# Performance work log

Measured on AMD Instinct MI355X. Metric: run time of the kernel, lower is better.

The kernel has to match this reference:

```python
import jax, jax.numpy as jnp
import numpy as np

B, T, H = 4, 2048, 1024
NH = 16
HD = H // NH  # 64
FF = 4 * H


def setup_inputs() -> dict:
    key = jax.random.key(0)
    ks = jax.random.split(key, 11)
    s = 0.02
    return {
        "x": jax.random.normal(ks[0], (B, T, H), dtype=jnp.float32),
        "Wq": jax.random.normal(ks[1], (H, H), dtype=jnp.float32) * s,
        "bq": jnp.zeros((H,), dtype=jnp.float32),
        "Wk": jax.random.normal(ks[2], (H, H), dtype=jnp.float32) * s,
        "bk": jnp.zeros((H,), dtype=jnp.float32),
        "Wv": jax.random.normal(ks[3], (H, H), dtype=jnp.float32) * s,
        "bv": jnp.zeros((H,), dtype=jnp.float32),
        "W1": jax.random.normal(ks[4], (H, FF), dtype=jnp.float32) * s,
        "b1": jnp.zeros((FF,), dtype=jnp.float32),
        "W2": jax.random.normal(ks[5], (FF, H), dtype=jnp.float32) * s,
        "b2": jnp.zeros((H,), dtype=jnp.float32),
    }


def _block(x, Wq, bq, Wk, bk, Wv, bv, W1, b1, W2, b2):
    b, t, h = x.shape
    # multi-head masked self-attention; NOTE: scale = full h_dim ** 0.5 (as in source)
    q = (x @ Wq + bq).reshape(b, t, NH, HD).transpose(0, 2, 1, 3)  # [B,nH,T,HD]
    k = (x @ Wk + bk).reshape(b, t, NH, HD).transpose(0, 2, 1, 3)
    v = (x @ Wv + bv).reshape(b, t, NH, HD).transpose(0, 2, 1, 3)
    att = jnp.einsum("bnqd,bnkd->bnqk", q, k) / (h ** 0.5)  # [B,nH,T,T]
    causal = jnp.tril(jnp.ones((t, t), dtype=bool))
    att = jnp.where(causal, att, -jnp.inf)
    w = jax.nn.softmax(att, axis=-1)
    attn_out = jnp.einsum("bnqk,bnkd->bnqd", w, v).transpose(0, 2, 1, 3).reshape(b, t, h)
    x = x + attn_out
    # MLP (dropout p=0 -> identity)
    mlp = jax.nn.gelu(x @ W1 + b1) @ W2 + b2
    return x + mlp


def reference(x, Wq, bq, Wk, bk, Wv, bv, W1, b1, W2, b2):
    return _block(x, Wq, bq, Wk, bk, Wv, bv, W1, b1, W2, b2)
```

## Files before the change

kernel.cpp:

```cpp
#include <hip/hip_runtime.h>
#include <cstdint>
#include <cstddef>

typedef unsigned short u16;
typedef __attribute__((ext_vector_type(8))) __bf16 bf16x8;
typedef __attribute__((ext_vector_type(4))) __bf16 bf16x4;
typedef __attribute__((ext_vector_type(4))) float f32x4;
typedef __attribute__((ext_vector_type(4))) u16 u16x4;

#define MFMA(a, b, c) __builtin_amdgcn_mfma_f32_16x16x32_bf16((a), (b), (c), 0, 0, 0)

__device__ __forceinline__ u16 f2b(float f) {
  union { __bf16 h; u16 u; } v;
  v.h = (__bf16)f;
  return v.u;
}

__device__ __forceinline__ void gld16(const void* g, void* l) {
  __builtin_amdgcn_global_load_lds(
      (__attribute__((address_space(1))) void*)(void*)(g),
      (__attribute__((address_space(3))) void*)(l), 16, 0, 0);
}

__device__ __forceinline__ size_t qk_off(int t, int hd) {
  return (size_t)((((t >> 4) * 2 + (hd >> 5)) * 512)
                  + ((((hd >> 3) & 3) * 16 + (t & 15)) * 8) + (hd & 7));
}
__device__ __forceinline__ size_t v_off(int t, int hd) {
  int kk = ((t & 15) << 2) | ((t >> 4) & 3);
  return (size_t)(((t >> 6) * 4096)
                  + (((hd >> 4) * 2 + (kk >> 5)) * 512)
                  + ((((kk >> 3) & 3) * 16 + (hd & 15)) * 8) + (kk & 7));
}

__global__ void xconv(const float* __restrict__ in, u16* __restrict__ out, int n) {
  int i = (blockIdx.x * blockDim.x + threadIdx.x) * 4;
  if (i >= n) return;
  float4 v = *(const float4*)(in + i);
  u16x4 o;
  o[0] = f2b(v.x); o[1] = f2b(v.y); o[2] = f2b(v.z); o[3] = f2b(v.w);
  *(u16x4*)(out + i) = o;
}

__global__ void wtrans_all(const float* __restrict__ Wq, const float* __restrict__ Wk,
                           const float* __restrict__ Wv, const float* __restrict__ W1,
                           const float* __restrict__ W2, u16* __restrict__ Wqkvt,
                           u16* __restrict__ W1t, u16* __restrict__ W2t) {
  __shared__ float tile[32][33];
  int blk = blockIdx.x;
  const float* W;
  u16* Wt;
  int Kd, Nd, nx;
  if (blk < 3072) {
    int s = blk >> 10;
    blk &= 1023;
    W = (s == 0) ? Wq : (s == 1) ? Wk : Wv;
    Wt = Wqkvt + (size_t)s * 1048576;
    Kd = 1024; Nd = 1024; nx = 32;
  } else if (blk < 7168) {
    blk -= 3072; W = W1; Wt = W1t; Kd = 1024; Nd = 4096; nx = 128;
  } else {
    blk -= 7168; W = W2; Wt = W2t; Kd = 4096; Nd = 1024; nx = 32;
  }
  int n0 = (blk % nx) * 32, k0 = (blk / nx) * 32;
  int tx = threadIdx.x, ty = threadIdx.y;
#pragma unroll
  for (int i = 0; i < 4; i++)
    tile[ty + i * 8][tx] = W[(size_t)(k0 + ty + i * 8) * Nd + n0 + tx];
  __syncthreads();
#pragma unroll
  for (int i = 0; i < 4; i++)
    Wt[(size_t)(n0 + ty + i * 8) * Kd + k0 + tx] = f2b(tile[tx][ty + i * 8]);
}

template <int MODE>
__global__ __launch_bounds__(512, 2) void gemm256(
    const u16* __restrict__ A, const u16* __restrict__ Bt,
    const float* __restrict__ b0, const float* __restrict__ b1,
    const float* __restrict__ b2, void* __restrict__ outp,
    const float* __restrict__ resid, int N, int K, float scale) {
  __shared__ __attribute__((aligned(16))) u16 As_[3][16384];
  __shared__ __attribute__((aligned(16))) u16 Bs_[3][8192];
  const int tid = threadIdx.x;
  const int wid = tid >> 6, lane = tid & 63;
  const int g = lane >> 4, r = lane & 15;

  const int xcd = blockIdx.x & 7;
  const int ii = blockIdx.x >> 3;
  const int bm = xcd * 4 + ((ii & 31) >> 3);
  const int bn = (ii >> 5) * 8 + (ii & 7);

  const int wrow = (wid >> 1) * 64;
  const int wcol = (wid & 1) * 64;

  const int ko0 = ((0 * 4 + g) ^ (r & 7)) * 8;
  const int ko1 = ((1 * 4 + g) ^ (r & 7)) * 8;

  size_t aOff[4], bOff[2];
#pragma unroll
  for (int i4 = 0; i4 < 4; i4++) {
    int cc = i4 * 512 + tid, row = cc >> 3;
    int js = ((cc & 7) ^ (row & 7)) * 8;
    aOff[i4] = (size_t)(bm * 256 + row) * K + js;
  }
#pragma unroll
  for (int i2 = 0; i2 < 2; i2++) {
    int cc = i2 * 512 + tid, row = cc >> 3;
    int js = ((cc & 7) ^ (row & 7)) * 8;
    bOff[i2] = (size_t)(bn * 128 + row) * K + js;
  }

  f32x4 acc[4][4];
  const f32x4 zero4 = {0.f, 0.f, 0.f, 0.f};
#pragma unroll
  for (int i = 0; i < 4; i++)
#pragma unroll
    for (int j = 0; j < 4; j++) acc[i][j] = zero4;

#pragma unroll
  for (int i4 = 0; i4 < 4; i4++) gld16(A + aOff[i4], &As_[0][(i4 * 512 + tid) * 8]);
#pragma unroll
  for (int i2 = 0; i2 < 2; i2++) gld16(Bt + bOff[i2], &Bs_[0][(i2 * 512 + tid) * 8]);
#pragma unroll
  for (int i4 = 0; i4 < 4; i4++) gld16(A + aOff[i4] + 64, &As_[1][(i4 * 512 + tid) * 8]);
#pragma unroll
  for (int i2 = 0; i2 < 2; i2++) gld16(Bt + bOff[i2] + 64, &Bs_[1][(i2 * 512 + tid) * 8]);
  asm volatile("s_waitcnt vmcnt(6)" ::: "memory");
  __builtin_amdgcn_s_barrier();

  const int KT = K >> 6;
  int cur = 0;
  for (int t = 0; t < KT; ++t) {
    const u16* as = As_[cur];
    const u16* bs = Bs_[cur];
    const int stg = (cur == 0) ? 2 : cur - 1;
    const bool more = (t + 2) < KT;
    const size_t k2 = (size_t)(t + 2) * 64;

    bf16x8 af0[4], bf0[4], af1[4], bf1[4];
#pragma unroll
    for (int mt = 0; mt < 4; mt++) {
      af0[mt] = *(const bf16x8*)&as[(wrow + mt * 16 + r) * 64 + ko0];
      af1[mt] = *(const bf16x8*)&as[(wrow + mt * 16 + r) * 64 + ko1];
    }
#pragma unroll
    for (int nt = 0; nt < 4; nt++) {
      bf0[nt] = *(const bf16x8*)&bs[(wcol + nt * 16 + r) * 64 + ko0];
      bf1[nt] = *(const bf16x8*)&bs[(wcol + nt * 16 + r) * 64 + ko1];
    }

    if (more) {
#pragma unroll
      for (int i4 = 0; i4 < 4; i4++)
        gld16(A + aOff[i4] + k2, &As_[stg][(i4 * 512 + tid) * 8]);
#pragma unroll
      for (int i2 = 0; i2 < 2; i2++)
        gld16(Bt + bOff[i2] + k2, &Bs_[stg][(i2 * 512 + tid) * 8]);
    }

#pragma unroll
    for (int mt = 0; mt < 4; mt++)
#pragma unroll
      for (int nt = 0; nt < 4; nt++)
        acc[mt][nt] = MFMA(af0[mt], bf0[nt], acc[mt][nt]);
#pragma unroll
    for (int mt = 0; mt < 4; mt++)
#pragma unroll
      for (int nt = 0; nt < 4; nt++)
        acc[mt][nt] = MFMA(af1[mt], bf1[nt], acc[mt][nt]);

    if (t + 1 < KT) {
      if (more) asm volatile("s_waitcnt vmcnt(6)" ::: "memory");
      else      asm volatile("s_waitcnt vmcnt(0)" ::: "memory");
    }
    __builtin_amdgcn_s_barrier();
    cur = (cur == 2) ? 0 : cur + 1;
  }

#pragma unroll
  for (int mt = 0; mt < 4; mt++) {
#pragma unroll
    for (int nt = 0; nt < 4; nt++) {
      int col = bn * 128 + wcol + nt * 16 + r;
      float bv;
      if (MODE == 4) {
        int sec = col >> 10, hcol = col & 1023;
        bv = (sec == 0) ? b0[hcol] : (sec == 1) ? b1[hcol] : b2[hcol];
      } else {
        bv = b0[col];
      }
#pragma unroll
      for (int q = 0; q < 4; q++) {
        int row = bm * 256 + wrow + mt * 16 + g * 4 + q;
        float v = acc[mt][nt][q] + bv;
        if (MODE == 2) {
          const float c1 = -2.3025850929940457f;
          const float c2 = c1 * 0.044715f;
          float t2 = v * v;
          float z = v * (c1 + c2 * t2);
          float sg = 1.0f / (1.0f + __builtin_amdgcn_exp2f(z));
          ((u16*)outp)[(size_t)row * N + col] = f2b(v * sg);
        } else if (MODE == 3) {
          ((float*)outp)[(size_t)row * N + col] = v + resid[(size_t)row * N + col];
        } else if (MODE == 4) {
          int sec = col >> 10, hcol = col & 1023;
          int head = hcol >> 6, hd = hcol & 63;
          int bb = row >> 11, tt = row & 2047;
          size_t hbase = ((size_t)bb * 16 + head) * 131072;
          u16* qout = (u16*)outp;
          if (sec == 0) {
            qout[hbase + qk_off(tt, hd)] = f2b(v * scale);
          } else if (sec == 1) {
            (qout + 8388608)[hbase + qk_off(tt, hd)] = f2b(v);
          } else {
            (qout + 16777216)[hbase + v_off(tt, hd)] = f2b(v);
          }
        }
      }
    }
  }
}

__global__ __launch_bounds__(256) void attn_kernel(
    const u16* __restrict__ Q, const u16* __restrict__ Kc,
    const u16* __restrict__ Vt, const float* __restrict__ x,
    float* __restrict__ x1, u16* __restrict__ xb1) {
  const int bh = blockIdx.x & 63;
  const int slot = blockIdx.x >> 6;
  const int tid = threadIdx.x;
  const int wid = tid >> 6, lane = tid & 63;
  const int g = lane >> 4, c = lane & 15;
  const u16* Qh = Q + (size_t)bh * 131072;
  const u16* Kh = Kc + (size_t)bh * 131072;
  const u16* Vh = Vt + (size_t)bh * 131072;
  const int b = bh >> 4, head = bh & 15;

  __shared__ __attribute__((aligned(16))) u16 Ks[8192];
  __shared__ __attribute__((aligned(16))) u16 Vs[8192];
  __shared__ __attribute__((aligned(16))) u16 P[4][32][72];

  bf16x8 ones;
#pragma unroll
  for (int i = 0; i < 8; i++) ones[i] = (__bf16)1.0f;

  const f32x4 zero4 = {0.f, 0.f, 0.f, 0.f};

  for (int phase = 0; phase < 2; ++phase) {
    const int bt = phase ? (15 - slot) : slot;
    const int q0b = bt * 128;
    const int q0 = q0b + wid * 32;
    const int kendw = q0 + 32;
    const int nkt = bt + 1;

    bf16x8 qf[2][2];
#pragma unroll
    for (int mt = 0; mt < 2; mt++)
#pragma unroll
      for (int h = 0; h < 2; h++)
        qf[mt][h] = *(const bf16x8*)&Qh[(((q0 >> 4) + mt) * 2 + h) * 512 + lane * 8];

    f32x4 o[2][4];
    f32x4 lac[2];
#pragma unroll
    for (int mt = 0; mt < 2; mt++) {
      lac[mt] = zero4;
#pragma unroll
      for (int i = 0; i < 4; i++) o[mt][i] = zero4;
    }

    for (int kt = 0; kt < nkt; ++kt) {
      const int k0 = kt * 128;
#pragma unroll
      for (int r2 = 0; r2 < 4; r2++) {
        int idx = (r2 * 256 + tid) * 8;
        gld16(Kh + (size_t)k0 * 64 + idx, Ks + idx);
        gld16(Vh + (size_t)k0 * 64 + idx, Vs + idx);
      }
      __syncthreads();

#pragma unroll
      for (int s2 = 0; s2 < 2; ++s2) {
        const int k0s = k0 + s2 * 64;
        if (k0s < kendw) {
          bf16x8 kf[4][2], vf[4][2];
#pragma unroll
          for (int nt = 0; nt < 4; nt++)
#pragma unroll
            for (int h = 0; h < 2; h++) {
              kf[nt][h] = *(const bf16x8*)&Ks[s2 * 4096 + (nt * 2 + h) * 512 + lane * 8];
              vf[nt][h] = *(const bf16x8*)&Vs[s2 * 4096 + (nt * 2 + h) * 512 + lane * 8];
            }

          f32x4 sv[2][4];
#pragma unroll
          for (int mt = 0; mt < 2; mt++)
#pragma unroll
            for (int nt = 0; nt < 4; nt++) sv[mt][nt] = zero4;
#pragma unroll
          for (int nt = 0; nt < 4; nt++)
#pragma unroll
            for (int mt = 0; mt < 2; mt++) {
              sv[mt][nt] = MFMA(qf[mt][0], kf[nt][0], sv[mt][nt]);
              sv[mt][nt] = MFMA(qf[mt][1], kf[nt][1], sv[mt][nt]);
            }

          if (k0s + 64 > q0) {
#pragma unroll
            for (int mt = 0; mt < 2; mt++)
#pragma unroll
              for (int rr = 0; rr < 4; rr++) {
                int q = q0 + mt * 16 + g * 4 + rr;
#pragma unroll
                for (int nt = 0; nt < 4; nt++)
                  if (k0s + nt * 16 + c > q) sv[mt][nt][rr] = -1e30f;
              }
          }

#pragma unroll
          for (int mt = 0; mt < 2; mt++)
#pragma unroll
            for (int rr = 0; rr < 4; rr++) {
              union { u16x4 u; bf16x4 h; } pw;
#pragma unroll
              for (int nt = 0; nt < 4; nt++)
                pw.h[nt] = (__bf16)__builtin_amdgcn_exp2f(sv[mt][nt][rr]);
              *(u16x4*)&P[wid][mt * 16 + g * 4 + rr][4 * c] = pw.u;
            }

          asm volatile("s_waitcnt lgkmcnt(0)" ::: "memory");

#pragma unroll
          for (int mt = 0; mt < 2; mt++) {
            bf16x8 pf0 = *(const bf16x8*)&P[wid][mt * 16 + c][g * 8];
            bf16x8 pf1 = *(const bf16x8*)&P[wid][mt * 16 + c][32 + g * 8];
            lac[mt] = MFMA(pf0, ones, lac[mt]);
            lac[mt] = MFMA(pf1, ones, lac[mt]);
#pragma unroll
            for (int ot = 0; ot < 4; ot++) {
              f32x4 oo = MFMA(pf0, vf[ot][0], o[mt][ot]);
              o[mt][ot] = MFMA(pf1, vf[ot][1], oo);
            }
          }
        }
      }
      __syncthreads();
    }

    float inv[2][4];
#pragma unroll
    for (int mt = 0; mt < 2; mt++)
#pragma unroll
      for (int rr = 0; rr < 4; rr++) inv[mt][rr] = 1.0f / lac[mt][rr];
#pragma unroll
    for (int mt = 0; mt < 2; mt++)
#pragma unroll
      for (int ot = 0; ot < 4; ot++)
#pragma unroll
        for (int rr = 0; rr < 4; rr++) {
          int t = q0 + mt * 16 + g * 4 + rr;
          int hd = ot * 16 + c;
          size_t xi = ((size_t)b * 2048 + t) * 1024 + head * 64 + hd;
          float v = x[xi] + o[mt][ot][rr] * inv[mt][rr];
          x1[xi] = v;
          xb1[xi] = f2b(v);
        }
  }
}

extern "C" void kernel_launch(void* const* d_in, const int* in_sizes, int n_in,
                              void* d_out, int out_size, void* d_ws, size_t ws_size,
                              hipStream_t stream) {
  (void)in_sizes; (void)n_in; (void)out_size; (void)ws_size;
  const float* x = (const float*)d_in[0];
  const float* Wq = (const float*)d_in[1];
  const float* bq = (const float*)d_in[2];
  const float* Wk = (const float*)d_in[3];
  const float* bk = (const float*)d_in[4];
  const float* Wv = (const float*)d_in[5];
  const float* bv = (const float*)d_in[6];
  const float* W1 = (const float*)d_in[7];
  const float* b1 = (const float*)d_in[8];
  const float* W2 = (const float*)d_in[9];
  const float* b2 = (const float*)d_in[10];

  char* ws = (char*)d_ws;
  size_t off = 0;
  auto alloc = [&](size_t bytes) {
    char* p = ws + off;
    off += (bytes + 255) & ~(size_t)255;
    return p;
  };
  u16* xb    = (u16*)alloc(8192ull * 1024 * 2);
  u16* Wqkvt = (u16*)alloc(3072ull * 1024 * 2);
  u16* W1t   = (u16*)alloc(4096ull * 1024 * 2);
  u16* W2t   = (u16*)alloc(1024ull * 4096 * 2);
  u16* Qb    = (u16*)alloc(3ull * 8192 * 1024 * 2);
  float* x1  = (float*)alloc(8192ull * 1024 * 4);
  u16* hb    = (u16*)alloc(8192ull * 4096 * 2);
  u16* xb1   = xb;
  u16* Kb    = Qb + 8388608;
  u16* Vtb   = Qb + 16777216;

  const float qscale = 1.4426950408889634f / 32.0f;

  xconv<<<dim3(8192), dim3(256), 0, stream>>>(x, xb, 8192 * 1024);
  wtrans_all<<<dim3(11264), dim3(32, 8), 0, stream>>>(
      Wq, Wk, Wv, W1, W2, Wqkvt, W1t, W2t);
  gemm256<4><<<dim3(768), dim3(512), 0, stream>>>(
      xb, Wqkvt, bq, bk, bv, Qb, nullptr, 3072, 1024, qscale);
  attn_kernel<<<dim3(512), dim3(256), 0, stream>>>(Qb, Kb, Vtb, x, x1, xb1);
  gemm256<2><<<dim3(1024), dim3(512), 0, stream>>>(
      xb1, W1t, b1, nullptr, nullptr, hb, nullptr, 4096, 1024, 1.0f);
  gemm256<3><<<dim3(256), dim3(512), 0, stream>>>(
      hb, W2t, b2, nullptr, nullptr, d_out, x1, 1024, 4096, 1.0f);
}
```

Baseline: 429.3 us.

## Use 256x256 tiles with double buffering for QKV and W1 GEMMs

Adds a gemm_big kernel with 256x256 output tiles per block (8 waves, each computing 128x64) instead of 256x128, halving the block count for the QKV and MLP-up GEMMs. Each block reuses more of every loaded A and B tile, which cuts LDS and global traffic per FLOP. The three-stage prefetch is replaced by two-stage double buffering, with the next A and B loads issued between the two k-halves. The trade-offs are more accumulator registers (128 per thread), less prefetch depth, a full vmcnt(0) wait each iteration, and fewer blocks to fill the CUs. The W2 GEMM keeps the old kernel.

```diff
diff --git a/kernel.cpp b/kernel.cpp
--- a/kernel.cpp
+++ b/kernel.cpp
@@ -74,58 +74,51 @@
 }
 
 template <int MODE>
-__global__ __launch_bounds__(512, 2) void gemm256(
+__global__ __launch_bounds__(512, 2) void gemm_big(
     const u16* __restrict__ A, const u16* __restrict__ Bt,
     const float* __restrict__ b0, const float* __restrict__ b1,
     const float* __restrict__ b2, void* __restrict__ outp,
-    const float* __restrict__ resid, int N, int K, float scale) {
-  __shared__ __attribute__((aligned(16))) u16 As_[3][16384];
-  __shared__ __attribute__((aligned(16))) u16 Bs_[3][8192];
+    int N, int K, float scale) {
+  __shared__ __attribute__((aligned(16))) u16 As_[2][16384];
+  __shared__ __attribute__((aligned(16))) u16 Bs_[2][16384];
   const int tid = threadIdx.x;
   const int wid = tid >> 6, lane = tid & 63;
   const int g = lane >> 4, r = lane & 15;
 
   const int xcd = blockIdx.x & 7;
   const int ii = blockIdx.x >> 3;
-  const int bm = xcd * 4 + ((ii & 31) >> 3);
-  const int bn = (ii >> 5) * 8 + (ii & 7);
-
-  const int wrow = (wid >> 1) * 64;
-  const int wcol = (wid & 1) * 64;
+  const int c4 = ii >> 4, w = ii & 15;
+  const int bm = xcd * 4 + (w >> 2);
+  const int bn = c4 * 4 + (w & 3);
+
+  const int wrow = (wid >> 2) * 128;
+  const int wcol = (wid & 3) * 64;
 
   const int ko0 = ((0 * 4 + g) ^ (r & 7)) * 8;
   const int ko1 = ((1 * 4 + g) ^ (r & 7)) * 8;
 
-  size_t aOff[4], bOff[2];
+  size_t aOff[4], bOff[4];
 #pragma unroll
   for (int i4 = 0; i4 < 4; i4++) {
     int cc = i4 * 512 + tid, row = cc >> 3;
     int js = ((cc & 7) ^ (row & 7)) * 8;
     aOff[i4] = (size_t)(bm * 256 + row) * K + js;
-  }
-#pragma unroll
-  for (int i2 = 0; i2 < 2; i2++) {
-    int cc = i2 * 512 + tid, row = cc >> 3;
-    int js = ((cc & 7) ^ (row & 7)) * 8;
-    bOff[i2] = (size_t)(bn * 128 + row) * K + js;
-  }
-
-  f32x4 acc[4][4];
+    bOff[i4] = (size_t)(bn * 256 + row) * K + js;
+  }
+
+  f32x4 acc[8][4];
   const f32x4 zero4 = {0.f, 0.f, 0.f, 0.f};
 #pragma unroll
-  for (int i = 0; i < 4; i++)
+  for (int i = 0; i < 8; i++)
 #pragma unroll
     for (int j = 0; j < 4; j++) acc[i][j] = zero4;
 
 #pragma unroll
-  for (int i4 = 0; i4 < 4; i4++) gld16(A + aOff[i4], &As_[0][(i4 * 512 + tid) * 8]);
-#pragma unroll
-  for (int i2 = 0; i2 < 2; i2++) gld16(Bt + bOff[i2], &Bs_[0][(i2 * 512 + tid) * 8]);
-#pragma unroll
-  for (int i4 = 0; i4 < 4; i4++) gld16(A + aOff[i4] + 64, &As_[1][(i4 * 512 + tid) * 8]);
-#pragma unroll
-  for (int i2 = 0; i2 < 2; i2++) gld16(Bt + bOff[i2] + 64, &Bs_[1][(i2 * 512 + tid) * 8]);
-  asm volatile("s_waitcnt vmcnt(6)" ::: "memory");
+  for (int i4 = 0; i4 < 4; i4++) {
+    gld16(A + aOff[i4], &As_[0][(i4 * 512 + tid) * 8]);
+    gld16(Bt + bOff[i4], &Bs_[0][(i4 * 512 + tid) * 8]);
+  }
+  asm volatile("s_waitcnt vmcnt(0)" ::: "memory");
   __builtin_amdgcn_s_barrier();
 
   const int KT = K >> 6;
@@ -133,55 +126,64 @@
   for (int t = 0; t < KT; ++t) {
     const u16* as = As_[cur];
     const u16* bs = Bs_[cur];
-    const int stg = (cur == 0) ? 2 : cur - 1;
-    const bool more = (t + 2) < KT;
-    const size_t k2 = (size_t)(t + 2) * 64;
-
-    bf16x8 af0[4], bf0[4], af1[4], bf1[4];
-#pragma unroll
-    for (int mt = 0; mt < 4; mt++) {
-      af0[mt] = *(const bf16x8*)&as[(wrow + mt * 16 + r) * 64 + ko0];
-      af1[mt] = *(const bf16x8*)&as[(wrow + mt * 16 + r) * 64 + ko1];
-    }
+    const int nxt = cur ^ 1;
+    const bool more = (t + 1) < KT;
+    const size_t k1 = (size_t)(t + 1) * 64;
+
+    if (more) {
+#pragma unroll
+      for (int i4 = 0; i4 < 4; i4++)
+        gld16(A + aOff[i4] + k1, &As_[nxt][(i4 * 512 + tid) * 8]);
+    }
+
+    {
+      bf16x8 af[8], bf[4];
+#pragma unroll
+      for (int mt = 0; mt < 8; mt++)
+        af[mt] = *(const bf16x8*)&as[(wrow + mt * 16 + r) * 64 + ko0];
+#pragma unroll
+      for (int nt = 0; nt < 4; nt++)
+        bf[nt] = *(const bf16x8*)&bs[(wcol + nt * 16 + r) * 64 + ko0];
+#pragma unroll
+      for (int mt = 0; mt < 8; mt++)
+#pragma unroll
+        for (int nt = 0; nt < 4; nt++)
+          acc[mt][nt] = MFMA(af[mt], bf[nt], acc[mt][nt]);
+    }
+
+    if (more) {
+#pragma unroll
+      for (int i4 = 0; i4 < 4; i4++)
+        gld16(Bt + bOff[i4] + k1, &Bs_[nxt][(i4 * 512 + tid) * 8]);
+    }
+
+    {
+      bf16x8 af[8], bf[4];
+#pragma unroll
+      for (int mt = 0; mt < 8; mt++)
+        af[mt] = *(const bf16x8*)&as[(wrow + mt * 16 + r) * 64 + ko1];
+#pragma unroll
+      for (int nt = 0; nt < 4; nt++)
+        bf[nt] = *(const bf16x8*)&bs[(wcol + nt * 16 + r) * 64 + ko1];
+#pragma unroll
+      for (int mt = 0; mt < 8; mt++)
+#pragma unroll
+        for (int nt = 0; nt < 4; nt++)
+          acc[mt][nt] = MFMA(af[mt], bf[nt], acc[mt][nt]);
+    }
+
+    if (more) {
+      asm volatile("s_waitcnt vmcnt(0)" ::: "memory");
+      __builtin_amdgcn_s_barrier();
+    }
+    cur = nxt;
+  }
+
+#pragma unroll
+  for (int mt = 0; mt < 8; mt++) {
 #pragma unroll
     for (int nt = 0; nt < 4; nt++) {
-      bf0[nt] = *(const bf16x8*)&bs[(wcol + nt * 16 + r) * 64 + ko0];
-      bf1[nt] = *(const bf16x8*)&bs[(wcol + nt * 16 + r) * 64 + ko1];
-    }
-
-    if (more) {
-#pragma unroll
-      for (int i4 = 0; i4 < 4; i4++)
-        gld16(A + aOff[i4] + k2, &As_[stg][(i4 * 512 + tid) * 8]);
-#pragma unroll
-      for (int i2 = 0; i2 < 2; i2++)
-        gld16(Bt + bOff[i2] + k2, &Bs_[stg][(i2 * 512 + tid) * 8]);
-    }
-
-#pragma unroll
-    for (int mt = 0; mt < 4; mt++)
-#pragma unroll
-      for (int nt = 0; nt < 4; nt++)
-        acc[mt][nt] = MFMA(af0[mt], bf0[nt], acc[mt][nt]);
-#pragma unroll
-    for (int mt = 0; mt < 4; mt++)
-#pragma unroll
-      for (int nt = 0; nt < 4; nt++)
-        acc[mt][nt] = MFMA(af1[mt], bf1[nt], acc[mt][nt]);
-
-    if (t + 1 < KT) {
-      if (more) asm volatile("s_waitcnt vmcnt(6)" ::: "memory");
-      else      asm volatile("s_waitcnt vmcnt(0)" ::: "memory");
-    }
-    __builtin_amdgcn_s_barrier();
-    cur = (cur == 2) ? 0 : cur + 1;
-  }
-
-#pragma unroll
-  for (int mt = 0; mt < 4; mt++) {
-#pragma unroll
-    for (int nt = 0; nt < 4; nt++) {
-      int col = bn * 128 + wcol + nt * 16 + r;
+      int col = bn * 256 + wcol + nt * 16 + r;
       float bv;
       if (MODE == 4) {
         int sec = col >> 10, hcol = col & 1023;
@@ -200,8 +202,6 @@
           float z = v * (c1 + c2 * t2);
           float sg = 1.0f / (1.0f + __builtin_amdgcn_exp2f(z));
           ((u16*)outp)[(size_t)row * N + col] = f2b(v * sg);
-        } else if (MODE == 3) {
-          ((float*)outp)[(size_t)row * N + col] = v + resid[(size_t)row * N + col];
         } else if (MODE == 4) {
           int sec = col >> 10, hcol = col & 1023;
           int head = hcol >> 6, hd = hcol & 63;
@@ -215,6 +215,127 @@
           } else {
             (qout + 16777216)[hbase + v_off(tt, hd)] = f2b(v);
           }
+        }
+      }
+    }
+  }
+}
+
+template <int MODE>
+__global__ __launch_bounds__(512, 2) void gemm256(
+    const u16* __restrict__ A, const u16* __restrict__ Bt,
+    const float* __restrict__ b0, void* __restrict__ outp,
+    const float* __restrict__ resid, int N, int K) {
+  __shared__ __attribute__((aligned(16))) u16 As_[3][16384];
+  __shared__ __attribute__((aligned(16))) u16 Bs_[3][8192];
+  const int tid = threadIdx.x;
+  const int wid = tid >> 6, lane = tid & 63;
+  const int g = lane >> 4, r = lane & 15;
+
+  const int xcd = blockIdx.x & 7;
+  const int ii = blockIdx.x >> 3;
+  const int bm = xcd * 4 + ((ii & 31) >> 3);
+  const int bn = (ii >> 5) * 8 + (ii & 7);
+
+  const int wrow = (wid >> 1) * 64;
+  const int wcol = (wid & 1) * 64;
+
+  const int ko0 = ((0 * 4 + g) ^ (r & 7)) * 8;
+  const int ko1 = ((1 * 4 + g) ^ (r & 7)) * 8;
+
+  size_t aOff[4], bOff[2];
+#pragma unroll
+  for (int i4 = 0; i4 < 4; i4++) {
+    int cc = i4 * 512 + tid, row = cc >> 3;
+    int js = ((cc & 7) ^ (row & 7)) * 8;
+    aOff[i4] = (size_t)(bm * 256 + row) * K + js;
+  }
+#pragma unroll
+  for (int i2 = 0; i2 < 2; i2++) {
+    int cc = i2 * 512 + tid, row = cc >> 3;
+    int js = ((cc & 7) ^ (row & 7)) * 8;
+    bOff[i2] = (size_t)(bn * 128 + row) * K + js;
+  }
+
+  f32x4 acc[4][4];
+  const f32x4 zero4 = {0.f, 0.f, 0.f, 0.f};
+#pragma unroll
+  for (int i = 0; i < 4; i++)
+#pragma unroll
+    for (int j = 0; j < 4; j++) acc[i][j] = zero4;
+
+#pragma unroll
+  for (int i4 = 0; i4 < 4; i4++) gld16(A + aOff[i4], &As_[0][(i4 * 512 + tid) * 8]);
+#pragma unroll
+  for (int i2 = 0; i2 < 2; i2++) gld16(Bt + bOff[i2], &Bs_[0][(i2 * 512 + tid) * 8]);
+#pragma unroll
+  for (int i4 = 0; i4 < 4; i4++) gld16(A + aOff[i4] + 64, &As_[1][(i4 * 512 + tid) * 8]);
+#pragma unroll
+  for (int i2 = 0; i2 < 2; i2++) gld16(Bt + bOff[i2] + 64, &Bs_[1][(i2 * 512 + tid) * 8]);
+  asm volatile("s_waitcnt vmcnt(6)" ::: "memory");
+  __builtin_amdgcn_s_barrier();
+
+  const int KT = K >> 6;
+  int cur = 0;
+  for (int t = 0; t < KT; ++t) {
+    const u16* as = As_[cur];
+    const u16* bs = Bs_[cur];
+    const int stg = (cur == 0) ? 2 : cur - 1;
+    const bool more = (t + 2) < KT;
+    const size_t k2 = (size_t)(t + 2) * 64;
+
+    bf16x8 af0[4], bf0[4], af1[4], bf1[4];
+#pragma unroll
+    for (int mt = 0; mt < 4; mt++) {
+      af0[mt] = *(const bf16x8*)&as[(wrow + mt * 16 + r) * 64 + ko0];
+      af1[mt] = *(const bf16x8*)&as[(wrow + mt * 16 + r) * 64 + ko1];
+    }
+#pragma unroll
+    for (int nt = 0; nt < 4; nt++) {
+      bf0[nt] = *(const bf16x8*)&bs[(wcol + nt * 16 + r) * 64 + ko0];
+      bf1[nt] = *(const bf16x8*)&bs[(wcol + nt * 16 + r) * 64 + ko1];
+    }
+
+    if (more) {
+#pragma unroll
+      for (int i4 = 0; i4 < 4; i4++)
+        gld16(A + aOff[i4] + k2, &As_[stg][(i4 * 512 + tid) * 8]);
+#pragma unroll
+      for (int i2 = 0; i2 < 2; i2++)
+        gld16(Bt + bOff[i2] + k2, &Bs_[stg][(i2 * 512 + tid) * 8]);
+    }
+
+#pragma unroll
+    for (int mt = 0; mt < 4; mt++)
+#pragma unroll
+      for (int nt = 0; nt < 4; nt++)
+        acc[mt][nt] = MFMA(af0[mt], bf0[nt], acc[mt][nt]);
+#pragma unroll
+    for (int mt = 0; mt < 4; mt++)
+#pragma unroll
+      for (int nt = 0; nt < 4; nt++)
+        acc[mt][nt] = MFMA(af1[mt], bf1[nt], acc[mt][nt]);
+
+    if (t + 1 < KT) {
+      if (more) asm volatile("s_waitcnt vmcnt(6)" ::: "memory");
+      else      asm volatile("s_waitcnt vmcnt(0)" ::: "memory");
+    }
+    __builtin_amdgcn_s_barrier();
+    cur = (cur == 2) ? 0 : cur + 1;
+  }
+
+#pragma unroll
+  for (int mt = 0; mt < 4; mt++) {
+#pragma unroll
+    for (int nt = 0; nt < 4; nt++) {
+      int col = bn * 128 + wcol + nt * 16 + r;
+      float bv = b0[col];
+#pragma unroll
+      for (int q = 0; q < 4; q++) {
+        int row = bm * 256 + wrow + mt * 16 + g * 4 + q;
+        float v = acc[mt][nt][q] + bv;
+        if (MODE == 3) {
+          ((float*)outp)[(size_t)row * N + col] = v + resid[(size_t)row * N + col];
         }
       }
     }
@@ -406,11 +527,11 @@
   xconv<<<dim3(8192), dim3(256), 0, stream>>>(x, xb, 8192 * 1024);
   wtrans_all<<<dim3(11264), dim3(32, 8), 0, stream>>>(
       Wq, Wk, Wv, W1, W2, Wqkvt, W1t, W2t);
-  gemm256<4><<<dim3(768), dim3(512), 0, stream>>>(
-      xb, Wqkvt, bq, bk, bv, Qb, nullptr, 3072, 1024, qscale);
+  gemm_big<4><<<dim3(384), dim3(512), 0, stream>>>(
+      xb, Wqkvt, bq, bk, bv, Qb, 3072, 1024, qscale);
   attn_kernel<<<dim3(512), dim3(256), 0, stream>>>(Qb, Kb, Vtb, x, x1, xb1);
-  gemm256<2><<<dim3(1024), dim3(512), 0, stream>>>(
-      xb1, W1t, b1, nullptr, nullptr, hb, nullptr, 4096, 1024, 1.0f);
+  gemm_big<2><<<dim3(512), dim3(512), 0, stream>>>(
+      xb1, W1t, b1, nullptr, nullptr, hb, 4096, 1024, 1.0f);
   gemm256<3><<<dim3(256), dim3(512), 0, stream>>>(
-      hb, W2t, b2, nullptr, nullptr, d_out, x1, 1024, 4096, 1.0f);
-}
+      hb, W2t, b2, d_out, x1, 1024, 4096);
+}
```

Measured after the change: 438.9 us. 2.2% more time.
